# Optimization experiments

Measured on AMD Instinct MI355X. Metric: run time of the kernel, lower is better.

## Reference

```python
import jax, jax.numpy as jnp
import numpy as np

N, E = 20000, 100000
D_IN, H1, C1 = 512, 8, 64   # conv1: 512 -> 8 heads x 64, concat -> 512
H2, C2 = 4, 128             # conv2: 512 -> 4 heads x 128, mean -> 128


def setup_inputs() -> dict:
    key = jax.random.key(0)
    k = jax.random.split(key, 12)
    s_in = 1.0 / np.sqrt(D_IN).astype(np.float32)
    return {
        "street_embedding": jax.random.normal(k[0], (N, D_IN), jnp.float32),
        "edge_index": jax.random.randint(k[1], (2, E), 0, N),
        "y": jax.random.randint(k[2], (N,), 0, C2),
        "train_mask": jax.random.bernoulli(k[3], 0.5, (N,)),
        "W1": jax.random.normal(k[4], (D_IN, H1 * C1), jnp.float32) * s_in,
        "att_src1": jax.random.normal(k[5], (H1, C1), jnp.float32) * 0.1,
        "att_dst1": jax.random.normal(k[6], (H1, C1), jnp.float32) * 0.1,
        "b1": jnp.zeros((H1 * C1,), jnp.float32),
        "W2": jax.random.normal(k[7], (H1 * C1, H2 * C2), jnp.float32) * s_in,
        "att_src2": jax.random.normal(k[8], (H2, C2), jnp.float32) * 0.1,
        "att_dst2": jax.random.normal(k[9], (H2, C2), jnp.float32) * 0.1,
        "b2": jnp.zeros((C2,), jnp.float32),
    }


def _gat_conv(x, W, a_src, a_dst, b, src, dst, n, H, C, concat):
    # linear transform (no bias, as in PyG GATConv's internal lin)
    xp = (x @ W).reshape(n, H, C)                      # [N,H,C]
    asrc = jnp.einsum('nhc,hc->nh', xp, a_src)         # [N,H]
    adst = jnp.einsum('nhc,hc->nh', xp, a_dst)
    e = jax.nn.leaky_relu(asrc[src] + adst[dst], 0.2)  # [E',H] edge scores
    # softmax over incoming edges per destination node
    m = jax.lax.stop_gradient(jax.ops.segment_max(e, dst, num_segments=n))
    ex = jnp.exp(e - m[dst])
    denom = jax.ops.segment_sum(ex, dst, num_segments=n)
    alpha = ex / (denom[dst] + 1e-16)                  # [E',H]
    out = jax.ops.segment_sum(alpha[:, :, None] * xp[src], dst, num_segments=n)  # [N,H,C]
    if concat:
        return out.reshape(n, H * C) + b
    return out.mean(axis=1) + b


def reference(street_embedding, edge_index, y, train_mask,
              W1, att_src1, att_dst1, b1, W2, att_src2, att_dst2, b2):
    n = street_embedding.shape[0]
    loop = jnp.arange(n)
    # PyG GATConv adds self-loops by default
    src = jnp.concatenate([edge_index[0], loop])
    dst = jnp.concatenate([edge_index[1], loop])
    # dropout layers are identity in eval mode
    h = _gat_conv(street_embedding, W1, att_src1, att_dst1, b1, src, dst, n, H1, C1, True)
    h = jax.nn.elu(h)
    out = _gat_conv(h, W2, att_src2, att_dst2, b2, src, dst, n, H2, C2, False)  # [N,C2]
    # CrossEntropyLoss, mean over train_mask nodes (weighted mean, jit-safe)
    logp = jax.nn.log_softmax(out, axis=-1)
    ce = -jnp.take_along_axis(logp, y[:, None], axis=-1)[:, 0]
    w = train_mask.astype(out.dtype)
    loss_su = jnp.sum(w * ce) / jnp.sum(w)
    return (loss_su, out)
```

## Files before the change

kernel.cpp:

```cpp
#include <hip/hip_runtime.h>
#include <cmath>

#define D_IN 512
#define HC   512
#define NH1  8
#define NC1  64
#define NH2  4
#define NC2  128
#define BM 128
#define BN 128
#define BK 32

typedef __attribute__((ext_vector_type(8))) short short8;
typedef __attribute__((ext_vector_type(4))) float f32x4;

__device__ inline ushort f2bf(float f) {
  unsigned u = __float_as_uint(f);
  return (ushort)((u + 0x7FFFu + ((u >> 16) & 1u)) >> 16);
}
__device__ inline float bf2f(ushort b) { return __uint_as_float(((unsigned)b) << 16); }

__global__ void k_cast(const float* __restrict__ in, ushort* __restrict__ outp, int n4) {
  int i = blockIdx.x * blockDim.x + threadIdx.x;
  if (i >= n4) return;
  float4 v = ((const float4*)in)[i];
  ushort4 r = { f2bf(v.x), f2bf(v.y), f2bf(v.z), f2bf(v.w) };
  ((ushort4*)outp)[i] = r;
}

__global__ void k_castT2(const float* __restrict__ W1, const float* __restrict__ W2,
                         ushort* __restrict__ Wt1, ushort* __restrict__ Wt2) {
  int idx = blockIdx.x * blockDim.x + threadIdx.x;
  const int KN = D_IN * HC;
  if (idx >= 2 * KN) return;
  const float* W = (idx < KN) ? W1 : W2;
  ushort* Wt = (idx < KN) ? Wt1 : Wt2;
  int i = (idx < KN) ? idx : idx - KN;
  int n = i / D_IN, k = i - n * D_IN;
  Wt[i] = f2bf(W[(size_t)k * HC + n]);
}

template<int H>
__global__ void k_gemm_bf16(const ushort* __restrict__ A, const ushort* __restrict__ Bt,
                            ushort* __restrict__ Cbf,
                            const float* __restrict__ att_s, const float* __restrict__ att_d,
                            float* __restrict__ asrc, float* __restrict__ adst, int M) {
  constexpr int C = HC / H;
  __shared__ __align__(16) ushort As[2][BM * BK];
  __shared__ __align__(16) ushort Bs[2][BN * BK];
  int t = threadIdx.x;
  int m0 = blockIdx.y * BM;
  int n0 = blockIdx.x * BN;
  int wave = t >> 6, lane = t & 63;
  int ln = lane & 15, qd = lane >> 4;
  int wm = (wave >> 1) * 64, wn = (wave & 1) * 64;

  f32x4 acc[4][4] = {};

  int g = t >> 6, ct = (t >> 4) & 3, lt = t & 15;
  int rA0 = m0 + g * 16 + lt;      if (rA0 > M - 1) rA0 = M - 1;
  int rA1 = m0 + 64 + g * 16 + lt; if (rA1 > M - 1) rA1 = M - 1;
  const ushort* gA0 = A + (size_t)rA0 * D_IN + ct * 8;
  const ushort* gA1 = A + (size_t)rA1 * D_IN + ct * 8;
  const ushort* gB0 = Bt + (size_t)(n0 + g * 16 + lt) * D_IN + ct * 8;
  const ushort* gB1 = Bt + (size_t)(n0 + 64 + g * 16 + lt) * D_IN + ct * 8;

#define ISSUE_TILE(k0, buf)                                                              \
  do {                                                                                   \
    __builtin_amdgcn_global_load_lds(                                                    \
        (const __attribute__((address_space(1))) void*)(gA0 + (k0)),                     \
        (__attribute__((address_space(3))) void*)(As[buf] + t * 8), 16, 0, 0);           \
    __builtin_amdgcn_global_load_lds(                                                    \
        (const __attribute__((address_space(1))) void*)(gA1 + (k0)),                     \
        (__attribute__((address_space(3))) void*)(As[buf] + 2048 + t * 8), 16, 0, 0);    \
    __builtin_amdgcn_global_load_lds(                                                    \
        (const __attribute__((address_space(1))) void*)(gB0 + (k0)),                     \
        (__attribute__((address_space(3))) void*)(Bs[buf] + t * 8), 16, 0, 0);           \
    __builtin_amdgcn_global_load_lds(                                                    \
        (const __attribute__((address_space(1))) void*)(gB1 + (k0)),                     \
        (__attribute__((address_space(3))) void*)(Bs[buf] + 2048 + t * 8), 16, 0, 0);    \
  } while (0)

  ISSUE_TILE(0, 0);

  for (int ks = 0; ks < 16; ++ks) {
    __syncthreads();
    if (ks < 15) ISSUE_TILE((ks + 1) * BK, (ks + 1) & 1);
    int b = ks & 1;
    short8 a[4], bb[4];
#pragma unroll
    for (int i = 0; i < 4; ++i)
      a[i] = *(const short8*)&As[b][(((wave >> 1) * 4 + i) * 4 + qd) * 128 + ln * 8];
#pragma unroll
    for (int j = 0; j < 4; ++j)
      bb[j] = *(const short8*)&Bs[b][(((wave & 1) * 4 + j) * 4 + qd) * 128 + ln * 8];
#pragma unroll
    for (int i = 0; i < 4; ++i)
#pragma unroll
      for (int j = 0; j < 4; ++j)
        acc[i][j] = __builtin_amdgcn_mfma_f32_16x16x32_bf16(a[i], bb[j], acc[i][j], 0, 0, 0);
  }
#undef ISSUE_TILE

#pragma unroll
  for (int i = 0; i < 4; ++i) {
#pragma unroll
    for (int reg = 0; reg < 4; ++reg) {
      int row = m0 + wm + i * 16 + qd * 4 + reg;
      if (row >= M) continue;
#pragma unroll
      for (int j = 0; j < 4; ++j)
        Cbf[(size_t)row * HC + n0 + wn + j * 16 + ln] = f2bf(acc[i][j][reg]);
    }
  }

  int colbase = n0 + wn;
  int h = colbase / C;
  float sa[4], da[4];
#pragma unroll
  for (int j = 0; j < 4; ++j) {
    int c = (colbase % C) + j * 16 + ln;
    sa[j] = att_s[h * C + c];
    da[j] = att_d[h * C + c];
  }
#pragma unroll
  for (int i = 0; i < 4; ++i) {
#pragma unroll
    for (int reg = 0; reg < 4; ++reg) {
      float ps = acc[i][0][reg] * sa[0] + acc[i][1][reg] * sa[1]
               + acc[i][2][reg] * sa[2] + acc[i][3][reg] * sa[3];
      float pd = acc[i][0][reg] * da[0] + acc[i][1][reg] * da[1]
               + acc[i][2][reg] * da[2] + acc[i][3][reg] * da[3];
#pragma unroll
      for (int o = 1; o < 16; o <<= 1) { ps += __shfl_xor(ps, o); pd += __shfl_xor(pd, o); }
      int row = m0 + wm + i * 16 + qd * 4 + reg;
      if (ln == 0 && row < M) {
        if (C == 64) { asrc[row * H + h] = ps; adst[row * H + h] = pd; }
        else { atomicAdd(&asrc[row * H + h], ps); atomicAdd(&adst[row * H + h], pd); }
      }
    }
  }
}

__global__ void k_hist(const int* __restrict__ ei, int E, int Etot, int* __restrict__ cnt) {
  int e = blockIdx.x * blockDim.x + threadIdx.x;
  if (e >= Etot) return;
  int d = (e < E) ? ei[E + e] : e - E;
  atomicAdd(&cnt[d], 1);
}

__global__ void k_scan(const int* __restrict__ cnt, int* __restrict__ rowstart, int N) {
  int tid = threadIdx.x;
  int T = (N + 1023) / 1024;
  int base = tid * T;
  int sum = 0;
  for (int i = 0; i < T; ++i) { int j = base + i; if (j < N) sum += cnt[j]; }
  int lane = tid & 63, w = tid >> 6;
  int v = sum;
#pragma unroll
  for (int off = 1; off < 64; off <<= 1) {
    int u = __shfl_up(v, off);
    if (lane >= off) v += u;
  }
  __shared__ int wsum[16];
  if (lane == 63) wsum[w] = v;
  __syncthreads();
  if (tid < 16) {
    int tv = wsum[tid];
#pragma unroll
    for (int off = 1; off < 16; off <<= 1) {
      int u = __shfl_up(tv, off);
      if (tid >= off) tv += u;
    }
    wsum[tid] = tv;
  }
  __syncthreads();
  int wave_prefix = (w == 0) ? 0 : wsum[w - 1];
  int run = wave_prefix + v - sum;
  for (int i = 0; i < T; ++i) {
    int j = base + i;
    if (j < N) { rowstart[j] = run; run += cnt[j]; }
  }
  if (tid == 1023) rowstart[N] = run;
}

__global__ void k_scatter(const int* __restrict__ ei, int E, int Etot,
                          const int* __restrict__ rowstart, int* __restrict__ cursor,
                          int* __restrict__ csr_src) {
  int e = blockIdx.x * blockDim.x + threadIdx.x;
  if (e >= Etot) return;
  int s = (e < E) ? ei[e] : e - E;
  int d = (e < E) ? ei[E + e] : e - E;
  int pos = atomicAdd(&cursor[d], 1);
  csr_src[rowstart[d] + pos] = s;
}

template<int H, int MODE>
__global__ void k_agg(const int* __restrict__ rowstart, const int* __restrict__ csr_src,
                      const float* __restrict__ asrc, const float* __restrict__ adst,
                      const ushort* __restrict__ xp, ushort* __restrict__ hout,
                      float* __restrict__ out2, const float* __restrict__ bias,
                      const int* __restrict__ y, const int* __restrict__ msk,
                      float* __restrict__ acc2, int N) {
  int n = blockIdx.x;
  int tid = threadIdx.x;
  constexpr int C = HC / H;
  int h = (tid * 4) / C;
  int beg = rowstart[n], end = rowstart[n + 1];

  __shared__ int   s_src[32];
  __shared__ float s_out[512];

  float adn = adst[n * H + h];
  float ax = 0.f, ay = 0.f, az = 0.f, aw = 0.f, wsum = 0.f;

  for (int c0 = beg; c0 < end; c0 += 32) {
    int len = end - c0; if (len > 32) len = 32;
    __syncthreads();
    if (tid < len) s_src[tid] = csr_src[c0 + tid];
    __syncthreads();
    int i = 0;
    for (; i + 1 < len; i += 2) {
      int s0 = s_src[i], s1 = s_src[i + 1];
      float v0 = asrc[s0 * H + h] + adn;
      float v1 = asrc[s1 * H + h] + adn;
      ushort4 a0 = ((const ushort4*)xp)[(size_t)s0 * 128 + tid];
      ushort4 a1 = ((const ushort4*)xp)[(size_t)s1 * 128 + tid];
      v0 = (v0 > 0.f) ? v0 : 0.2f * v0;
      v1 = (v1 > 0.f) ? v1 : 0.2f * v1;
      float w0 = __expf(v0), w1 = __expf(v1);
      ax += w0 * bf2f(a0.x) + w1 * bf2f(a1.x);
      ay += w0 * bf2f(a0.y) + w1 * bf2f(a1.y);
      az += w0 * bf2f(a0.z) + w1 * bf2f(a1.z);
      aw += w0 * bf2f(a0.w) + w1 * bf2f(a1.w);
      wsum += w0 + w1;
    }
    if (i < len) {
      int s0 = s_src[i];
      float v0 = asrc[s0 * H + h] + adn;
      ushort4 a0 = ((const ushort4*)xp)[(size_t)s0 * 128 + tid];
      v0 = (v0 > 0.f) ? v0 : 0.2f * v0;
      float w0 = __expf(v0);
      ax += w0 * bf2f(a0.x); ay += w0 * bf2f(a0.y);
      az += w0 * bf2f(a0.z); aw += w0 * bf2f(a0.w);
      wsum += w0;
    }
  }
  float rdn = 1.0f / (wsum + 1e-16f);
  ax *= rdn; ay *= rdn; az *= rdn; aw *= rdn;

  if (MODE == 1) {
    int hc = tid * 4;
    float v0 = ax + bias[hc], v1 = ay + bias[hc + 1];
    float v2 = az + bias[hc + 2], v3 = aw + bias[hc + 3];
    v0 = (v0 > 0.f) ? v0 : expm1f(v0);
    v1 = (v1 > 0.f) ? v1 : expm1f(v1);
    v2 = (v2 > 0.f) ? v2 : expm1f(v2);
    v3 = (v3 > 0.f) ? v3 : expm1f(v3);
    ushort4 rr = { f2bf(v0), f2bf(v1), f2bf(v2), f2bf(v3) };
    ((ushort4*)hout)[(size_t)n * 128 + tid] = rr;
  } else {
    int hc = tid * 4;
    s_out[hc] = ax; s_out[hc + 1] = ay; s_out[hc + 2] = az; s_out[hc + 3] = aw;
    __syncthreads();
    if (tid < 32) {
#pragma unroll
      for (int k = 0; k < 4; ++k) {
        int c = tid * 4 + k;
        float sum = s_out[c] + s_out[128 + c] + s_out[256 + c] + s_out[384 + c];
        float lg = sum * 0.25f + bias[c];
        out2[(size_t)n * NC2 + c] = lg;
        s_out[c] = lg;
      }
    }
    __syncthreads();
    float lv = s_out[tid];
    int lane = tid & 63, wv = tid >> 6;
    float mx = lv;
#pragma unroll
    for (int o = 32; o > 0; o >>= 1) mx = fmaxf(mx, __shfl_xor(mx, o));
    if (lane == 0) s_out[256 + wv] = mx;
    __syncthreads();
    mx = fmaxf(s_out[256], s_out[257]);
    float e = __expf(lv - mx);
#pragma unroll
    for (int o = 32; o > 0; o >>= 1) e += __shfl_xor(e, o);
    if (lane == 0) s_out[260 + wv] = e;
    __syncthreads();
    if (tid == 0 && msk[n] != 0) {
      float se = s_out[260] + s_out[261];
      float ce = mx + logf(se) - s_out[y[n]];
      int slot = n & 127;
      atomicAdd(&acc2[slot], ce);
      atomicAdd(&acc2[128 + slot], 1.0f);
    }
  }
}

__global__ void k_final(const float* __restrict__ acc2, float* __restrict__ out0) {
  int tid = threadIdx.x;
  float ce = acc2[tid], ct = acc2[128 + tid];
#pragma unroll
  for (int o = 32; o > 0; o >>= 1) { ce += __shfl_xor(ce, o); ct += __shfl_xor(ct, o); }
  __shared__ float s[4];
  if ((tid & 63) == 0) { s[(tid >> 6) * 2] = ce; s[(tid >> 6) * 2 + 1] = ct; }
  __syncthreads();
  if (tid == 0) out0[0] = (s[0] + s[2]) / (s[1] + s[3]);
}

extern "C" void kernel_launch(void* const* d_in, const int* in_sizes, int n_in,
                              void* d_out, int out_size, void* d_ws, size_t ws_size,
                              hipStream_t stream) {
  const float* x   = (const float*)d_in[0];
  const int*   ei  = (const int*)d_in[1];
  const int*   y   = (const int*)d_in[2];
  const int*   msk = (const int*)d_in[3];
  const float* W1  = (const float*)d_in[4];
  const float* as1 = (const float*)d_in[5];
  const float* ad1 = (const float*)d_in[6];
  const float* b1  = (const float*)d_in[7];
  const float* W2  = (const float*)d_in[8];
  const float* as2 = (const float*)d_in[9];
  const float* ad2 = (const float*)d_in[10];
  const float* b2  = (const float*)d_in[11];
  float* out = (float*)d_out;

  int N = in_sizes[0] / D_IN;
  int E = in_sizes[1] / 2;
  int Etot = E + N;

  float* ws = (float*)d_ws;
  size_t NF = (size_t)N * HC;
  float* asr1 = ws;
  float* adt1 = asr1 + (size_t)N * NH1;
  float* asr2 = adt1 + (size_t)N * NH1;
  float* adt2 = asr2 + (size_t)N * NH2;
  float* acc2 = adt2 + (size_t)N * NH2;
  int*   cnt    = (int*)(acc2 + 256);
  int*   cursor = cnt + N;
  size_t zero_bytes = ((size_t)N * 2 * NH2 + 256 + 2 * (size_t)N) * sizeof(float);
  int*   rowstart = cursor + N;
  int*   csr_src  = rowstart + N + 1;
  ushort* xpbf = (ushort*)((((uintptr_t)(csr_src + Etot)) + 15) & ~(uintptr_t)15);
  ushort* Abf = xpbf + NF;
  ushort* Wt1 = Abf + NF;
  ushort* Wt2 = Wt1 + (size_t)D_IN * HC;

  hipMemsetAsync(asr2, 0, zero_bytes, stream);

  k_castT2<<<(2 * D_IN * HC + 255) / 256, 256, 0, stream>>>(W1, W2, Wt1, Wt2);

  k_hist<<<(Etot + 255) / 256, 256, 0, stream>>>(ei, E, Etot, cnt);
  k_scan<<<1, 1024, 0, stream>>>(cnt, rowstart, N);
  k_scatter<<<(Etot + 255) / 256, 256, 0, stream>>>(ei, E, Etot, rowstart, cursor, csr_src);

  dim3 ggrid(HC / BN, (N + BM - 1) / BM);

  k_cast<<<(int)((NF / 4 + 255) / 256), 256, 0, stream>>>(x, Abf, (int)(NF / 4));
  k_gemm_bf16<NH1><<<ggrid, 256, 0, stream>>>(Abf, Wt1, xpbf, as1, ad1, asr1, adt1, N);
  k_agg<NH1, 1><<<N, 128, 0, stream>>>(rowstart, csr_src, asr1, adt1, xpbf, Abf,
                                       nullptr, b1, nullptr, nullptr, nullptr, N);

  k_gemm_bf16<NH2><<<ggrid, 256, 0, stream>>>(Abf, Wt2, xpbf, as2, ad2, asr2, adt2, N);
  k_agg<NH2, 2><<<N, 128, 0, stream>>>(rowstart, csr_src, asr2, adt2, xpbf, nullptr,
                                       out + 1, b2, y, msk, acc2, N);

  k_final<<<1, 128, 0, stream>>>(acc2, out);
}
```

Before: 300.2 us.

## Merge cast kernels, single-buffer GEMM with BK=64, drop attention atomics

Three separate changes. The x and weight cast/transpose kernels are merged into one launch. The GEMM's double-buffered BK=32 prefetch pipeline becomes a single buffer loaded with BK=64 and a sync before compute, which halves the number of barrier iterations but drops the overlap of loads with MFMA. Layer-2 attention scores are now written as two partial sums per head and added during aggregation, which removes the float atomics and most of the memset.

Result: faster. 287.8 us, median of 2 (-4.1%).

```diff
diff --git a/kernel.cpp b/kernel.cpp
--- a/kernel.cpp
+++ b/kernel.cpp
@@ -9,7 +9,7 @@
 #define NC2  128
 #define BM 128
 #define BN 128
-#define BK 32
+#define BK 64
 
 typedef __attribute__((ext_vector_type(8))) short short8;
 typedef __attribute__((ext_vector_type(4))) float f32x4;
@@ -20,24 +20,24 @@
 }
 __device__ inline float bf2f(ushort b) { return __uint_as_float(((unsigned)b) << 16); }
 
-__global__ void k_cast(const float* __restrict__ in, ushort* __restrict__ outp, int n4) {
+__global__ void k_cast_all(const float* __restrict__ x, ushort* __restrict__ Abf,
+                           const float* __restrict__ W1, const float* __restrict__ W2,
+                           ushort* __restrict__ Wt1, ushort* __restrict__ Wt2, int n4x) {
+  const int KN = D_IN * HC;
   int i = blockIdx.x * blockDim.x + threadIdx.x;
-  if (i >= n4) return;
-  float4 v = ((const float4*)in)[i];
-  ushort4 r = { f2bf(v.x), f2bf(v.y), f2bf(v.z), f2bf(v.w) };
-  ((ushort4*)outp)[i] = r;
-}
-
-__global__ void k_castT2(const float* __restrict__ W1, const float* __restrict__ W2,
-                         ushort* __restrict__ Wt1, ushort* __restrict__ Wt2) {
-  int idx = blockIdx.x * blockDim.x + threadIdx.x;
-  const int KN = D_IN * HC;
-  if (idx >= 2 * KN) return;
-  const float* W = (idx < KN) ? W1 : W2;
-  ushort* Wt = (idx < KN) ? Wt1 : Wt2;
-  int i = (idx < KN) ? idx : idx - KN;
-  int n = i / D_IN, k = i - n * D_IN;
-  Wt[i] = f2bf(W[(size_t)k * HC + n]);
+  if (i < n4x) {
+    float4 v = ((const float4*)x)[i];
+    ushort4 r = { f2bf(v.x), f2bf(v.y), f2bf(v.z), f2bf(v.w) };
+    ((ushort4*)Abf)[i] = r;
+  } else {
+    int idx = i - n4x;
+    if (idx >= 2 * KN) return;
+    const float* W = (idx < KN) ? W1 : W2;
+    ushort* Wt = (idx < KN) ? Wt1 : Wt2;
+    int j = (idx < KN) ? idx : idx - KN;
+    int n = j / D_IN, k = j - n * D_IN;
+    Wt[j] = f2bf(W[(size_t)k * HC + n]);
+  }
 }
 
 template<int H>
@@ -46,8 +46,8 @@
                             const float* __restrict__ att_s, const float* __restrict__ att_d,
                             float* __restrict__ asrc, float* __restrict__ adst, int M) {
   constexpr int C = HC / H;
-  __shared__ __align__(16) ushort As[2][BM * BK];
-  __shared__ __align__(16) ushort Bs[2][BN * BK];
+  __shared__ __align__(16) ushort As[BM * BK];
+  __shared__ __align__(16) ushort Bs[BN * BK];
   int t = threadIdx.x;
   int m0 = blockIdx.y * BM;
   int n0 = blockIdx.x * BN;
@@ -65,42 +65,43 @@
   const ushort* gB0 = Bt + (size_t)(n0 + g * 16 + lt) * D_IN + ct * 8;
   const ushort* gB1 = Bt + (size_t)(n0 + 64 + g * 16 + lt) * D_IN + ct * 8;
 
-#define ISSUE_TILE(k0, buf)                                                              \
-  do {                                                                                   \
-    __builtin_amdgcn_global_load_lds(                                                    \
-        (const __attribute__((address_space(1))) void*)(gA0 + (k0)),                     \
-        (__attribute__((address_space(3))) void*)(As[buf] + t * 8), 16, 0, 0);           \
-    __builtin_amdgcn_global_load_lds(                                                    \
-        (const __attribute__((address_space(1))) void*)(gA1 + (k0)),                     \
-        (__attribute__((address_space(3))) void*)(As[buf] + 2048 + t * 8), 16, 0, 0);    \
-    __builtin_amdgcn_global_load_lds(                                                    \
-        (const __attribute__((address_space(1))) void*)(gB0 + (k0)),                     \
-        (__attribute__((address_space(3))) void*)(Bs[buf] + t * 8), 16, 0, 0);           \
-    __builtin_amdgcn_global_load_lds(                                                    \
-        (const __attribute__((address_space(1))) void*)(gB1 + (k0)),                     \
-        (__attribute__((address_space(3))) void*)(Bs[buf] + 2048 + t * 8), 16, 0, 0);    \
-  } while (0)
-
-  ISSUE_TILE(0, 0);
-
-  for (int ks = 0; ks < 16; ++ks) {
-    __syncthreads();
-    if (ks < 15) ISSUE_TILE((ks + 1) * BK, (ks + 1) & 1);
-    int b = ks & 1;
-    short8 a[4], bb[4];
-#pragma unroll
-    for (int i = 0; i < 4; ++i)
-      a[i] = *(const short8*)&As[b][(((wave >> 1) * 4 + i) * 4 + qd) * 128 + ln * 8];
-#pragma unroll
-    for (int j = 0; j < 4; ++j)
-      bb[j] = *(const short8*)&Bs[b][(((wave & 1) * 4 + j) * 4 + qd) * 128 + ln * 8];
-#pragma unroll
-    for (int i = 0; i < 4; ++i)
+  for (int k0 = 0; k0 < D_IN; k0 += BK) {
+    __syncthreads();
+#pragma unroll
+    for (int h = 0; h < 2; ++h) {
+      int ko = k0 + h * 32;
+      int lo = h * 4096;
+      __builtin_amdgcn_global_load_lds(
+          (const __attribute__((address_space(1))) void*)(gA0 + ko),
+          (__attribute__((address_space(3))) void*)(As + lo + t * 8), 16, 0, 0);
+      __builtin_amdgcn_global_load_lds(
+          (const __attribute__((address_space(1))) void*)(gA1 + ko),
+          (__attribute__((address_space(3))) void*)(As + lo + 2048 + t * 8), 16, 0, 0);
+      __builtin_amdgcn_global_load_lds(
+          (const __attribute__((address_space(1))) void*)(gB0 + ko),
+          (__attribute__((address_space(3))) void*)(Bs + lo + t * 8), 16, 0, 0);
+      __builtin_amdgcn_global_load_lds(
+          (const __attribute__((address_space(1))) void*)(gB1 + ko),
+          (__attribute__((address_space(3))) void*)(Bs + lo + 2048 + t * 8), 16, 0, 0);
+    }
+    __syncthreads();
+#pragma unroll
+    for (int h = 0; h < 2; ++h) {
+      int lo = h * 4096;
+      short8 a[4], bb[4];
+#pragma unroll
+      for (int i = 0; i < 4; ++i)
+        a[i] = *(const short8*)&As[lo + (((wave >> 1) * 4 + i) * 4 + qd) * 128 + ln * 8];
 #pragma unroll
       for (int j = 0; j < 4; ++j)
-        acc[i][j] = __builtin_amdgcn_mfma_f32_16x16x32_bf16(a[i], bb[j], acc[i][j], 0, 0, 0);
-  }
-#undef ISSUE_TILE
+        bb[j] = *(const short8*)&Bs[lo + (((wave & 1) * 4 + j) * 4 + qd) * 128 + ln * 8];
+#pragma unroll
+      for (int i = 0; i < 4; ++i)
+#pragma unroll
+        for (int j = 0; j < 4; ++j)
+          acc[i][j] = __builtin_amdgcn_mfma_f32_16x16x32_bf16(a[i], bb[j], acc[i][j], 0, 0, 0);
+    }
+  }
 
 #pragma unroll
   for (int i = 0; i < 4; ++i) {
@@ -135,8 +136,13 @@
       for (int o = 1; o < 16; o <<= 1) { ps += __shfl_xor(ps, o); pd += __shfl_xor(pd, o); }
       int row = m0 + wm + i * 16 + qd * 4 + reg;
       if (ln == 0 && row < M) {
-        if (C == 64) { asrc[row * H + h] = ps; adst[row * H + h] = pd; }
-        else { atomicAdd(&asrc[row * H + h], ps); atomicAdd(&adst[row * H + h], pd); }
+        if (C == 64) {
+          asrc[row * H + h] = ps; adst[row * H + h] = pd;
+        } else {
+          int sub = (colbase >> 6) & 1;
+          asrc[(row * H + h) * 2 + sub] = ps;
+          adst[(row * H + h) * 2 + sub] = pd;
+        }
       }
     }
   }
@@ -211,8 +217,12 @@
   __shared__ int   s_src[32];
   __shared__ float s_out[512];
 
-  float adn = adst[n * H + h];
+  float adn = (MODE == 1) ? adst[n * H + h]
+                          : adst[(n * H + h) * 2] + adst[(n * H + h) * 2 + 1];
   float ax = 0.f, ay = 0.f, az = 0.f, aw = 0.f, wsum = 0.f;
+
+#define SCORE(s) ((MODE == 1) ? asrc[(s) * H + h] \
+                              : asrc[((s) * H + h) * 2] + asrc[((s) * H + h) * 2 + 1])
 
   for (int c0 = beg; c0 < end; c0 += 32) {
     int len = end - c0; if (len > 32) len = 32;
@@ -222,8 +232,8 @@
     int i = 0;
     for (; i + 1 < len; i += 2) {
       int s0 = s_src[i], s1 = s_src[i + 1];
-      float v0 = asrc[s0 * H + h] + adn;
-      float v1 = asrc[s1 * H + h] + adn;
+      float v0 = SCORE(s0) + adn;
+      float v1 = SCORE(s1) + adn;
       ushort4 a0 = ((const ushort4*)xp)[(size_t)s0 * 128 + tid];
       ushort4 a1 = ((const ushort4*)xp)[(size_t)s1 * 128 + tid];
       v0 = (v0 > 0.f) ? v0 : 0.2f * v0;
@@ -237,7 +247,7 @@
     }
     if (i < len) {
       int s0 = s_src[i];
-      float v0 = asrc[s0 * H + h] + adn;
+      float v0 = SCORE(s0) + adn;
       ushort4 a0 = ((const ushort4*)xp)[(size_t)s0 * 128 + tid];
       v0 = (v0 > 0.f) ? v0 : 0.2f * v0;
       float w0 = __expf(v0);
@@ -246,6 +256,7 @@
       wsum += w0;
     }
   }
+#undef SCORE
   float rdn = 1.0f / (wsum + 1e-16f);
   ax *= rdn; ay *= rdn; az *= rdn; aw *= rdn;
 
@@ -334,11 +345,11 @@
   float* asr1 = ws;
   float* adt1 = asr1 + (size_t)N * NH1;
   float* asr2 = adt1 + (size_t)N * NH1;
-  float* adt2 = asr2 + (size_t)N * NH2;
-  float* acc2 = adt2 + (size_t)N * NH2;
+  float* adt2 = asr2 + (size_t)N * 2 * NH2;
+  float* acc2 = adt2 + (size_t)N * 2 * NH2;
   int*   cnt    = (int*)(acc2 + 256);
   int*   cursor = cnt + N;
-  size_t zero_bytes = ((size_t)N * 2 * NH2 + 256 + 2 * (size_t)N) * sizeof(float);
+  size_t zero_bytes = (256 + 2 * (size_t)N) * sizeof(float);
   int*   rowstart = cursor + N;
   int*   csr_src  = rowstart + N + 1;
   ushort* xpbf = (ushort*)((((uintptr_t)(csr_src + Etot)) + 15) & ~(uintptr_t)15);
@@ -346,9 +357,11 @@
   ushort* Wt1 = Abf + NF;
   ushort* Wt2 = Wt1 + (size_t)D_IN * HC;
 
-  hipMemsetAsync(asr2, 0, zero_bytes, stream);
-
-  k_castT2<<<(2 * D_IN * HC + 255) / 256, 256, 0, stream>>>(W1, W2, Wt1, Wt2);
+  hipMemsetAsync(acc2, 0, zero_bytes, stream);
+
+  int n4x = (int)(NF / 4);
+  int cast_total = n4x + 2 * D_IN * HC;
+  k_cast_all<<<(cast_total + 255) / 256, 256, 0, stream>>>(x, Abf, W1, W2, Wt1, Wt2, n4x);
 
   k_hist<<<(Etot + 255) / 256, 256, 0, stream>>>(ei, E, Etot, cnt);
   k_scan<<<1, 1024, 0, stream>>>(cnt, rowstart, N);
@@ -356,7 +369,6 @@
 
   dim3 ggrid(HC / BN, (N + BM - 1) / BM);
 
-  k_cast<<<(int)((NF / 4 + 255) / 256), 256, 0, stream>>>(x, Abf, (int)(NF / 4));
   k_gemm_bf16<NH1><<<ggrid, 256, 0, stream>>>(Abf, Wt1, xpbf, as1, ad1, asr1, adt1, N);
   k_agg<NH1, 1><<<N, 128, 0, stream>>>(rowstart, csr_src, asr1, adt1, xpbf, Abf,
                                        nullptr, b1, nullptr, nullptr, nullptr, N);
```
